# Optimization experiments

Measured on AMD Instinct MI355X. Metric: run time of the kernel, lower is better.

## Reference

```python
import jax, jax.numpy as jnp
import numpy as np

H = 512; W = 512          # image size
K = 1024                  # fixed cap on points per cloud (original is data-dependent)
P = 8                     # n_points = n_points_rate * radius
R = 1.0                   # radius
THR = 5                   # point_threshould
LAM = 0.1                 # lam


def _lbp_uniform(img):
    """skimage-style uniform LBP, P=8, R=1, bilinear sampling (edge-clamped)."""
    Hh, Ww = img.shape
    rows = jnp.arange(Hh)
    cols = jnp.arange(Ww)
    bits = []
    for k in range(P):
        dr = float(np.round(-R * np.sin(2.0 * np.pi * k / P), 8))
        dc = float(np.round(R * np.cos(2.0 * np.pi * k / P), 8))
        rr = rows + dr
        cc = cols + dc
        r0 = jnp.floor(rr)
        c0 = jnp.floor(cc)
        fr = (rr - r0)[:, None]
        fc = (cc - c0)[None, :]
        r0i = jnp.clip(r0.astype(jnp.int32), 0, Hh - 1)
        r1i = jnp.clip(r0i + 1, 0, Hh - 1)
        c0i = jnp.clip(c0.astype(jnp.int32), 0, Ww - 1)
        c1i = jnp.clip(c0i + 1, 0, Ww - 1)
        g = lambda ri, ci: img[ri][:, ci]
        sample = ((1 - fr) * ((1 - fc) * g(r0i, c0i) + fc * g(r0i, c1i))
                  + fr * ((1 - fc) * g(r1i, c0i) + fc * g(r1i, c1i)))
        bits.append((sample - img >= 0).astype(jnp.int32))
    b = jnp.stack(bits)                                    # [P,H,W]
    changes = jnp.sum(jnp.abs(b - jnp.roll(b, 1, axis=0)), axis=0)
    s = jnp.sum(b, axis=0)
    return jnp.where(changes <= 2, s, P + 1).astype(jnp.float32)


def _select_points(mask2d):
    """Row-major coordinates of True pixels, zero-padded/truncated to K points."""
    flat = mask2d.reshape(-1)
    order = jnp.argsort(jnp.where(flat, 0, 1), stable=True)[:K]  # True pixels first, row-major
    valid = flat[order].astype(jnp.float32)
    r = (order // W).astype(jnp.float32)
    c = (order % W).astype(jnp.float32)
    return jnp.stack([r, c], axis=-1) * valid[:, None]     # [K,2]


def _pdist(x):
    sq = jnp.sum(x * x, axis=-1)
    d2 = sq[:, None] + sq[None, :] - 2.0 * (x @ x.T)
    return jnp.sqrt(jnp.maximum(d2, 0.0))


def _mst_pairing(D):
    """Prim's MST edges = dim-0 Vietoris-Rips persistence pairing. [K-1,2] int32."""
    N = D.shape[0]
    INF = jnp.float32(1e9)
    in_tree = jnp.zeros(N, bool).at[0].set(True)
    mind = D[0]
    src = jnp.zeros(N, jnp.int32)

    def step(carry, _):
        mind, src, in_tree = carry
        j = jnp.argmin(jnp.where(in_tree, INF, mind)).astype(jnp.int32)
        edge = jnp.stack([src[j], j])
        in_tree = in_tree.at[j].set(True)
        upd = (D[j] < mind) & ~in_tree
        mind = jnp.where(upd, D[j], mind)
        src = jnp.where(upd, j, src)
        return (mind, src, in_tree), edge

    _, edges = jax.lax.scan(step, (mind, src, in_tree), None, length=N - 1)
    return edges


def _sample_loss(pred_bin, mask_bin):
    pts_p = _select_points(_lbp_uniform(pred_bin) < THR)
    pts_m = _select_points(_lbp_uniform(mask_bin) < THR)
    Dp = _pdist(pts_p)
    Dm = _pdist(pts_m)
    ep = _mst_pairing(Dp)
    em = _mst_pairing(Dm)
    sig = lambda D, e: D[e[:, 0], e[:, 1]]
    l_p = jnp.linalg.norm(sig(Dp, ep) - sig(Dm, ep))   # signature of pred pairing
    l_m = jnp.linalg.norm(sig(Dp, em) - sig(Dm, em))   # signature of mask pairing
    return l_p + l_m


def setup_inputs() -> dict:
    key = jax.random.key(0)
    k1, k2, k3 = jax.random.split(key, 3)
    images = jax.random.normal(k1, (8, 1, H, W), dtype=jnp.float32)
    model_output = jax.random.normal(k2, (8, 1, H, W), dtype=jnp.float32)
    labels = jax.random.uniform(k3, (8, 1, H, W), dtype=jnp.float32)
    return {"images": images, "model_output": model_output, "labels": labels}


def reference(images, model_output, labels):
    preds = jax.nn.sigmoid(model_output[:, 0])          # squeeze channel dim
    masks = labels[:, 0]
    pred_bin = (preds > 0.5).astype(jnp.float32)
    mask_bin = (masks > 0.5).astype(jnp.float32)
    per_sample = jax.vmap(_sample_loss)(pred_bin, mask_bin)
    return LAM * jnp.sum(per_sample) / pred_bin.shape[0]
```

## Files before the change

kernel.cpp:

```cpp
#include <hip/hip_runtime.h>

#define HH 512
#define WW 512
#define NPIX (HH * WW)
#define NIMG 16
#define KPTS 1024
#define NWORDS (NPIX / 64)

__global__ void lbp_kernel(const float* __restrict__ mo,
                           const float* __restrict__ lb,
                           unsigned long long* __restrict__ maskbits) {
    int m = blockIdx.y;
    int pix = blockIdx.x * blockDim.x + threadIdx.x;
    int r = pix >> 9, c = pix & 511;
    int sample = m >> 1;
    const float* img = (m & 1) ? (lb + sample * NPIX) : (mo + sample * NPIX);
    float thr = (m & 1) ? 0.5f : 0.0f;

    int rm = r - (r > 0), rp = r + (r < HH - 1);
    int cm = c - (c > 0), cp = c + (c < WW - 1);
    const float* rowm = img + rm * WW;
    const float* row0 = img + r  * WW;
    const float* rowp = img + rp * WW;

    bool bmm = rowm[cm] > thr, bm0 = rowm[c] > thr, bmp = rowm[cp] > thr;
    bool b0m = row0[cm] > thr, b00 = row0[c] > thr, b0p = row0[cp] > thr;
    bool bpm = rowp[cm] > thr, bp0 = rowp[c] > thr, bpp = rowp[cp] > thr;

    bool r0e = (r == 0), c0e = (c == 0);
    bool t2m = r0e ? bpm : b0m;
    bool t2c = r0e ? bp0 : b00;
    bool t2p = r0e ? bpp : b0p;
    bool mc2 = c0e ? bmp : bm0;
    bool tc2 = c0e ? t2p : t2c;
    bool zc2 = c0e ? b0p : b00;
    bool pc2 = c0e ? bpp : bp0;

    unsigned bb =
        (b0p                     ?   1u : 0u)
      | ((bm0 & bmp & t2c & t2p) ?   2u : 0u)
      | (bm0                     ?   4u : 0u)
      | ((bmm & mc2 & t2m & tc2) ?   8u : 0u)
      | (b0m                     ?  16u : 0u)
      | ((b0m & zc2 & bpm & pc2) ?  32u : 0u)
      | (bp0                     ?  64u : 0u)
      | ((b0p & bp0 & bpp)       ? 128u : 0u);

    unsigned rol = ((bb << 1) | (bb >> 7)) & 0xFFu;
    int changes = __popc(bb ^ rol);
    int s = __popc(bb);
    bool maskbit = b00 && (changes <= 2) && (s < 5);

    unsigned long long w = __ballot(maskbit);
    if ((threadIdx.x & 63) == 0)
        maskbits[m * NWORDS + (pix >> 6)] = w;
}

__global__ void select_kernel(const unsigned long long* __restrict__ maskbits,
                              unsigned* __restrict__ ptsG) {
    __shared__ unsigned swv[4];
    int m = blockIdx.x, tid = threadIdx.x;
    int lane = tid & 63, wid = tid >> 6;

    for (int i = tid; i < KPTS; i += 256) ptsG[m * KPTS + i] = 0u;
    __syncthreads();

    unsigned running = 0;
    for (int ch = 0; ch < 16; ch++) {
        int w = ch * 256 + tid;
        unsigned long long word = maskbits[m * NWORDS + w];
        unsigned cnt = (unsigned)__popcll(word);

        unsigned x = cnt;
#pragma unroll
        for (int d = 1; d < 64; d <<= 1) {
            unsigned y = (unsigned)__shfl_up((int)x, d, 64);
            x += (lane >= d) ? y : 0u;
        }
        if (lane == 63) swv[wid] = x;
        __syncthreads();
        unsigned woff = 0, total = 0;
#pragma unroll
        for (int ww = 0; ww < 4; ww++) {
            unsigned t = swv[ww];
            total += t;
            woff += (ww < wid) ? t : 0u;
        }
        unsigned rank = running + woff + x - cnt;
        while (word) {
            int b = __builtin_ctzll(word);
            word &= word - 1;
            if (rank < (unsigned)KPTS) {
                unsigned p = (unsigned)(w * 64 + b);
                unsigned rr = p >> 9, cc = p & 511u;
                ptsG[m * KPTS + rank] = (rr << 16) | cc;
            }
            rank++;
        }
        running += total;
        if (running >= (unsigned)KPTS) break;
        __syncthreads();
    }
}

typedef short v2s __attribute__((ext_vector_type(2)));
typedef unsigned u32x4 __attribute__((ext_vector_type(4)));

__device__ __forceinline__ int dist2_packed(unsigned a, unsigned b) {
#if __has_builtin(__builtin_amdgcn_sdot2)
    v2s d = __builtin_bit_cast(v2s, a) - __builtin_bit_cast(v2s, b);
    return __builtin_amdgcn_sdot2(d, d, 0, false);
#else
    int dr = (int)(a >> 16) - (int)(b >> 16);
    int dc = (int)(a & 0xFFFFu) - (int)(b & 0xFFFFu);
    return __mul24(dr, dr) + __mul24(dc, dc);
#endif
}

template <int CTRL>
__device__ __forceinline__ unsigned umin_dpp(unsigned x) {
    unsigned o = (unsigned)__builtin_amdgcn_update_dpp((int)x, (int)x, CTRL,
                                                       0xf, 0xf, false);
    return o < x ? o : x;
}

__device__ __forceinline__ unsigned wave_min_to_lane63(unsigned x) {
    x = umin_dpp<0x111>(x);
    x = umin_dpp<0x112>(x);
    x = umin_dpp<0x114>(x);
    x = umin_dpp<0x118>(x);
    x = umin_dpp<0x142>(x);
    x = umin_dpp<0x143>(x);
    return x;
}

__device__ __forceinline__ unsigned umin3(unsigned a, unsigned b, unsigned c) {
    unsigned t = a < b ? a : b;
    return t < c ? t : c;
}

__device__ __forceinline__ unsigned mk_key(unsigned ps, unsigned qs, int izb) {
#if __has_builtin(__builtin_amdgcn_sdot2)
    v2s d = __builtin_bit_cast(v2s, ps) - __builtin_bit_cast(v2s, qs);
    return (unsigned)__builtin_amdgcn_sdot2(d, d, izb, false);
#else
    int dr = (int)(short)(ps >> 16) - (int)(short)(qs >> 16);
    int dc = (int)(short)(ps & 0xFFFFu) - (int)(short)(qs & 0xFFFFu);
    return (unsigned)(dr * dr + dc * dc + izb);
#endif
}

#define OSLOT_INIT(sl)                                                    \
    oi##sl = (((wid * 4 + sl) << 6) | lane) - 1024;       \
    oq##sl = base[((wid * 4 + sl) << 6) | lane] << 5;                     \
    ok##sl = mk_key(oq##sl, pt0s, oi##sl);

#define OSLOT_UPD(sl)                                                     \
    { unsigned _nk = mk_key(oq##sl, pjs, oi##sl);                         \
      ok##sl = (unsigned)min((int)ok##sl, (int)_nk); }

#define SEL16P(res)                                                       \
    { unsigned _a0 = b0 ? p1  : p0;                                       \
      unsigned _a1 = b0 ? p3  : p2;                                       \
      unsigned _a2 = b0 ? p5  : p4;                                       \
      unsigned _a3 = b0 ? p7  : p6;                                       \
      unsigned _a4 = b0 ? p9  : p8;                                       \
      unsigned _a5 = b0 ? p11 : p10;                                      \
      unsigned _a6 = b0 ? p13 : p12;                                      \
      unsigned _a7 = b0 ? p15 : p14;                                      \
      unsigned _c0 = b1 ? _a1 : _a0;                                      \
      unsigned _c1 = b1 ? _a3 : _a2;                                      \
      unsigned _c2 = b1 ? _a5 : _a4;                                      \
      unsigned _c3 = b1 ? _a7 : _a6;                                      \
      unsigned _e0 = b2 ? _c1 : _c0;                                      \
      unsigned _e1 = b2 ? _c3 : _c2;                                      \
      res = b3 ? _e1 : _e0; }

__global__ __launch_bounds__(256, 1) void mst_kernel(const unsigned* __restrict__ ptsG,
                                                     unsigned* __restrict__ edgesG) {
    __shared__ __align__(16) unsigned xmin[2][4];
    int tid = threadIdx.x;
    int lane = tid & 63, wid = tid >> 6;
    int m = blockIdx.x;
    const unsigned* base = ptsG + m * KPTS;
    unsigned pt0s = base[0] << 5;

    unsigned p0  = base[( 0 << 6) | lane] << 5;
    unsigned p1  = base[( 1 << 6) | lane] << 5;
    unsigned p2  = base[( 2 << 6) | lane] << 5;
    unsigned p3  = base[( 3 << 6) | lane] << 5;
    unsigned p4  = base[( 4 << 6) | lane] << 5;
    unsigned p5  = base[( 5 << 6) | lane] << 5;
    unsigned p6  = base[( 6 << 6) | lane] << 5;
    unsigned p7  = base[( 7 << 6) | lane] << 5;
    unsigned p8  = base[( 8 << 6) | lane] << 5;
    unsigned p9  = base[( 9 << 6) | lane] << 5;
    unsigned p10 = base[(10 << 6) | lane] << 5;
    unsigned p11 = base[(11 << 6) | lane] << 5;
    unsigned p12 = base[(12 << 6) | lane] << 5;
    unsigned p13 = base[(13 << 6) | lane] << 5;
    unsigned p14 = base[(14 << 6) | lane] << 5;
    unsigned p15 = base[(15 << 6) | lane] << 5;

    unsigned oq0, oq1, oq2, oq3;
    unsigned ok0, ok1, ok2, ok3;
    int      oi0, oi1, oi2, oi3;
    OSLOT_INIT(0); OSLOT_INIT(1); OSLOT_INIT(2); OSLOT_INIT(3);

    unsigned* eout = edgesG + m * KPTS;
    unsigned r3i = umin3(ok0, ok1, ok2);
    unsigned rk = r3i < ok3 ? r3i : ok3;

    unsigned acc = 0;
    int par = 0;

    for (int chk = 0; chk < 16; chk++) {
        int tmax = (chk < 15) ? 64 : 63;
        for (int t = 0; t < tmax; t++) {
            unsigned wmin = wave_min_to_lane63(rk);
            if (lane == 63) xmin[par][wid] = wmin;
            __syncthreads();

            u32x4 xv = *reinterpret_cast<const u32x4*>(&xmin[par][0]);
            unsigned vm = umin3(xv.x, xv.y, xv.z);
            vm = vm < xv.w ? vm : xv.w;
            unsigned wk = (unsigned)__builtin_amdgcn_readfirstlane((int)vm) + 1024u;
            par ^= 1;

            unsigned j = wk & 1023u;
            int wslot = (int)(j >> 6);
            int wlane = (int)(j & 63u);

            bool b0 = (wslot & 1) != 0, b1 = (wslot & 2) != 0;
            bool b2 = (wslot & 4) != 0, b3 = (wslot & 8) != 0;
            unsigned selPay;
            SEL16P(selPay);
            unsigned pjs = (unsigned)__builtin_amdgcn_readlane((int)selPay, wlane);

            acc = (lane == t) ? wk : acc;

            OSLOT_UPD(0); OSLOT_UPD(1); OSLOT_UPD(2); OSLOT_UPD(3);
            unsigned r3 = umin3(ok0, ok1, ok2);
            rk = r3 < ok3 ? r3 : ok3;
        }
        if (wid == 0) eout[(chk << 6) + lane] = acc;
    }
}

__global__ void recover_kernel(const unsigned* __restrict__ ptsG,
                               const unsigned* __restrict__ edgesG,
                               float* __restrict__ contrib) {
    __shared__ unsigned sS[KPTS];
    __shared__ unsigned sO[KPTS];
    __shared__ unsigned short sT[KPTS];
    int g = blockIdx.x, m = blockIdx.y;
    int tid = threadIdx.x;
    int partner = m ^ 1;

    for (int i = tid; i < KPTS; i += 256) {
        sS[i] = ptsG[m * KPTS + i];
        sO[i] = ptsG[partner * KPTS + i];
    }
    for (int e = tid; e < KPTS - 1; e += 256) {
        unsigned wkk = edgesG[m * KPTS + e];
        sT[wkk & 1023u] = (unsigned short)(e + 1);
    }
    if (tid == 0) sT[0] = 0;
    __syncthreads();

    int lane = tid & 63, w = tid >> 6;
    for (int k = 0; k < 16; k++) {
        int e = g * 64 + w * 16 + k;
        if (e >= KPTS - 1) break;
        unsigned wk = edgesG[m * KPTS + e];
        unsigned j = wk & 1023u;
        unsigned d2p = wk >> 10;
        unsigned pj = sS[j];
        unsigned te1 = (unsigned)(e + 1);

        unsigned best = 0xFFFFFFFFu;
#pragma unroll
        for (int i = 0; i < 16; i++) {
            int v = i * 64 + lane;
            unsigned pv = sS[v];
            int d2 = dist2_packed(pv, pj);
            unsigned tv1 = (unsigned)sT[v];
            bool qual = ((unsigned)d2 == d2p) && (tv1 < te1);
            unsigned cand = qual ? ((tv1 << 10) | (unsigned)v) : 0xFFFFFFFFu;
            best = cand < best ? cand : best;
        }
#pragma unroll
        for (int dd = 32; dd; dd >>= 1) {
            unsigned o = (unsigned)__shfl_xor((int)best, dd, 64);
            best = o < best ? o : best;
        }
        unsigned vsrc = best & 1023u;
        if (lane == 0) {
            unsigned oj = sO[j], os = sO[vsrc];
            float Dp = __fsqrt_rn((float)d2p);
            float Dm = __fsqrt_rn((float)dist2_packed(oj, os));
            float diff = Dp - Dm;
            contrib[m * (KPTS - 1) + e] = diff * diff;
        }
    }
}

__global__ void final_kernel(const float* __restrict__ contrib,
                             float* __restrict__ out) {
    __shared__ double part[NIMG];
    int t = threadIdx.x;
    if (t < NIMG) {
        double s = 0.0;
        for (int e = 0; e < KPTS - 1; e++)
            s += (double)contrib[t * (KPTS - 1) + e];
        part[t] = sqrt(s);
    }
    __syncthreads();
    if (t == 0) {
        double tot = 0.0;
        for (int i = 0; i < NIMG; i++) tot += part[i];
        out[0] = (float)(0.1 * tot / 8.0);
    }
}

extern "C" void kernel_launch(void* const* d_in, const int* in_sizes, int n_in,
                              void* d_out, int out_size, void* d_ws, size_t ws_size,
                              hipStream_t stream) {
    const float* mo = (const float*)d_in[1];
    const float* lb = (const float*)d_in[2];

    unsigned long long* maskbits = (unsigned long long*)d_ws;
    unsigned* edgesG = (unsigned*)d_ws;
    float* contrib = (float*)((char*)d_ws + (size_t)64 * 1024);
    unsigned* ptsG = (unsigned*)((char*)d_ws + (size_t)NIMG * NWORDS * 8);
    float* out = (float*)d_out;

    lbp_kernel<<<dim3(NPIX / 256, NIMG), 256, 0, stream>>>(mo, lb, maskbits);
    select_kernel<<<NIMG, 256, 0, stream>>>(maskbits, ptsG);
    mst_kernel<<<NIMG, 256, 0, stream>>>(ptsG, edgesG);
    recover_kernel<<<dim3(16, NIMG), 256, 0, stream>>>(ptsG, edgesG, contrib);
    final_kernel<<<1, 64, 0, stream>>>(contrib, out);
}
```

Before: 412.2 us.

## Interleave two independent Prim MST problems per block to hide barrier latency

Each MST block now runs the Prim iterations of two point clouds (pred and mask of one sample) in lockstep, with a single __syncthreads per pair of phases. Each phase reads the other cloud's reduction result that was published before the previous barrier. The serial per-step latency of the block-level min reduction, the barrier, and the readlane selection is meant to be overlapped with independent work from the second problem. The cost is twice the register state per thread and half as many blocks, which only matters if per-block throughput were the limit.

```diff
diff --git a/kernel.cpp b/kernel.cpp
--- a/kernel.cpp
+++ b/kernel.cpp
@@ -150,24 +150,15 @@
 #endif
 }
 
-#define OSLOT_INIT(sl)                                                    \
-    oi##sl = (((wid * 4 + sl) << 6) | lane) - 1024;       \
-    oq##sl = base[((wid * 4 + sl) << 6) | lane] << 5;                     \
-    ok##sl = mk_key(oq##sl, pt0s, oi##sl);
-
-#define OSLOT_UPD(sl)                                                     \
-    { unsigned _nk = mk_key(oq##sl, pjs, oi##sl);                         \
-      ok##sl = (unsigned)min((int)ok##sl, (int)_nk); }
-
-#define SEL16P(res)                                                       \
-    { unsigned _a0 = b0 ? p1  : p0;                                       \
-      unsigned _a1 = b0 ? p3  : p2;                                       \
-      unsigned _a2 = b0 ? p5  : p4;                                       \
-      unsigned _a3 = b0 ? p7  : p6;                                       \
-      unsigned _a4 = b0 ? p9  : p8;                                       \
-      unsigned _a5 = b0 ? p11 : p10;                                      \
-      unsigned _a6 = b0 ? p13 : p12;                                      \
-      unsigned _a7 = b0 ? p15 : p14;                                      \
+#define SEL16(P, res)                                                     \
+    { unsigned _a0 = b0 ? P##1  : P##0;                                   \
+      unsigned _a1 = b0 ? P##3  : P##2;                                   \
+      unsigned _a2 = b0 ? P##5  : P##4;                                   \
+      unsigned _a3 = b0 ? P##7  : P##6;                                   \
+      unsigned _a4 = b0 ? P##9  : P##8;                                   \
+      unsigned _a5 = b0 ? P##11 : P##10;                                  \
+      unsigned _a6 = b0 ? P##13 : P##12;                                  \
+      unsigned _a7 = b0 ? P##15 : P##14;                                  \
       unsigned _c0 = b1 ? _a1 : _a0;                                      \
       unsigned _c1 = b1 ? _a3 : _a2;                                      \
       unsigned _c2 = b1 ? _a5 : _a4;                                      \
@@ -176,74 +167,119 @@
       unsigned _e1 = b2 ? _c3 : _c2;                                      \
       res = b3 ? _e1 : _e0; }
 
+#define LOADP(P, B)                                                       \
+    unsigned P##0  = B[( 0 << 6) | lane] << 5;                            \
+    unsigned P##1  = B[( 1 << 6) | lane] << 5;                            \
+    unsigned P##2  = B[( 2 << 6) | lane] << 5;                            \
+    unsigned P##3  = B[( 3 << 6) | lane] << 5;                            \
+    unsigned P##4  = B[( 4 << 6) | lane] << 5;                            \
+    unsigned P##5  = B[( 5 << 6) | lane] << 5;                            \
+    unsigned P##6  = B[( 6 << 6) | lane] << 5;                            \
+    unsigned P##7  = B[( 7 << 6) | lane] << 5;                            \
+    unsigned P##8  = B[( 8 << 6) | lane] << 5;                            \
+    unsigned P##9  = B[( 9 << 6) | lane] << 5;                            \
+    unsigned P##10 = B[(10 << 6) | lane] << 5;                            \
+    unsigned P##11 = B[(11 << 6) | lane] << 5;                            \
+    unsigned P##12 = B[(12 << 6) | lane] << 5;                            \
+    unsigned P##13 = B[(13 << 6) | lane] << 5;                            \
+    unsigned P##14 = B[(14 << 6) | lane] << 5;                            \
+    unsigned P##15 = B[(15 << 6) | lane] << 5;
+
+#define MST_PHASE(P, OQ, OK, ACC, XI) do {                                \
+    u32x4 _xv = *reinterpret_cast<const u32x4*>(&xm[XI][par][0]);         \
+    unsigned _vm = umin3(_xv.x, _xv.y, _xv.z);                            \
+    _vm = _vm < _xv.w ? _vm : _xv.w;                                      \
+    unsigned _wk = (unsigned)__builtin_amdgcn_readfirstlane((int)_vm) + 1024u; \
+    unsigned _j = _wk & 1023u;                                            \
+    int _ws = (int)(_j >> 6), _wl = (int)(_j & 63u);                      \
+    bool b0 = (_ws & 1) != 0, b1 = (_ws & 2) != 0;                        \
+    bool b2 = (_ws & 4) != 0, b3 = (_ws & 8) != 0;                        \
+    unsigned _sel; SEL16(P, _sel);                                        \
+    unsigned _pjs = (unsigned)__builtin_amdgcn_readlane((int)_sel, _wl);  \
+    ACC = (lane == t) ? _wk : ACC;                                        \
+    { unsigned _nk = mk_key(OQ##0, _pjs, oi0);                            \
+      OK##0 = (unsigned)min((int)OK##0, (int)_nk); }                      \
+    { unsigned _nk = mk_key(OQ##1, _pjs, oi1);                            \
+      OK##1 = (unsigned)min((int)OK##1, (int)_nk); }                      \
+    { unsigned _nk = mk_key(OQ##2, _pjs, oi2);                            \
+      OK##2 = (unsigned)min((int)OK##2, (int)_nk); }                      \
+    { unsigned _nk = mk_key(OQ##3, _pjs, oi3);                            \
+      OK##3 = (unsigned)min((int)OK##3, (int)_nk); }                      \
+    unsigned _r3 = umin3(OK##0, OK##1, OK##2);                            \
+    unsigned _rk = _r3 < OK##3 ? _r3 : OK##3;                             \
+    unsigned _wm = wave_min_to_lane63(_rk);                               \
+    if (lane == 63) xm[XI][par ^ 1][wid] = _wm;                           \
+} while (0)
+
 __global__ __launch_bounds__(256, 1) void mst_kernel(const unsigned* __restrict__ ptsG,
                                                      unsigned* __restrict__ edgesG) {
-    __shared__ __align__(16) unsigned xmin[2][4];
+    __shared__ __align__(16) unsigned xm[2][2][4];
     int tid = threadIdx.x;
     int lane = tid & 63, wid = tid >> 6;
-    int m = blockIdx.x;
-    const unsigned* base = ptsG + m * KPTS;
-    unsigned pt0s = base[0] << 5;
-
-    unsigned p0  = base[( 0 << 6) | lane] << 5;
-    unsigned p1  = base[( 1 << 6) | lane] << 5;
-    unsigned p2  = base[( 2 << 6) | lane] << 5;
-    unsigned p3  = base[( 3 << 6) | lane] << 5;
-    unsigned p4  = base[( 4 << 6) | lane] << 5;
-    unsigned p5  = base[( 5 << 6) | lane] << 5;
-    unsigned p6  = base[( 6 << 6) | lane] << 5;
-    unsigned p7  = base[( 7 << 6) | lane] << 5;
-    unsigned p8  = base[( 8 << 6) | lane] << 5;
-    unsigned p9  = base[( 9 << 6) | lane] << 5;
-    unsigned p10 = base[(10 << 6) | lane] << 5;
-    unsigned p11 = base[(11 << 6) | lane] << 5;
-    unsigned p12 = base[(12 << 6) | lane] << 5;
-    unsigned p13 = base[(13 << 6) | lane] << 5;
-    unsigned p14 = base[(14 << 6) | lane] << 5;
-    unsigned p15 = base[(15 << 6) | lane] << 5;
-
-    unsigned oq0, oq1, oq2, oq3;
-    unsigned ok0, ok1, ok2, ok3;
-    int      oi0, oi1, oi2, oi3;
-    OSLOT_INIT(0); OSLOT_INIT(1); OSLOT_INIT(2); OSLOT_INIT(3);
-
-    unsigned* eout = edgesG + m * KPTS;
-    unsigned r3i = umin3(ok0, ok1, ok2);
-    unsigned rk = r3i < ok3 ? r3i : ok3;
-
-    unsigned acc = 0;
+    int b = blockIdx.x;
+    const unsigned* baseX = ptsG + (2 * b)     * KPTS;
+    const unsigned* baseY = ptsG + (2 * b + 1) * KPTS;
+    unsigned pt0sX = baseX[0] << 5;
+    unsigned pt0sY = baseY[0] << 5;
+
+    LOADP(pX, baseX)
+    LOADP(pY, baseY)
+
+    int oi0 = (((wid * 4 + 0) << 6) | lane) - 1024;
+    int oi1 = (((wid * 4 + 1) << 6) | lane) - 1024;
+    int oi2 = (((wid * 4 + 2) << 6) | lane) - 1024;
+    int oi3 = (((wid * 4 + 3) << 6) | lane) - 1024;
+
+    unsigned oqX0 = pX0, oqX1, oqX2, oqX3;
+    unsigned oqY0, oqY1, oqY2, oqY3;
+    oqX0 = baseX[((wid * 4 + 0) << 6) | lane] << 5;
+    oqX1 = baseX[((wid * 4 + 1) << 6) | lane] << 5;
+    oqX2 = baseX[((wid * 4 + 2) << 6) | lane] << 5;
+    oqX3 = baseX[((wid * 4 + 3) << 6) | lane] << 5;
+    oqY0 = baseY[((wid * 4 + 0) << 6) | lane] << 5;
+    oqY1 = baseY[((wid * 4 + 1) << 6) | lane] << 5;
+    oqY2 = baseY[((wid * 4 + 2) << 6) | lane] << 5;
+    oqY3 = baseY[((wid * 4 + 3) << 6) | lane] << 5;
+
+    unsigned okX0 = mk_key(oqX0, pt0sX, oi0);
+    unsigned okX1 = mk_key(oqX1, pt0sX, oi1);
+    unsigned okX2 = mk_key(oqX2, pt0sX, oi2);
+    unsigned okX3 = mk_key(oqX3, pt0sX, oi3);
+    unsigned okY0 = mk_key(oqY0, pt0sY, oi0);
+    unsigned okY1 = mk_key(oqY1, pt0sY, oi1);
+    unsigned okY2 = mk_key(oqY2, pt0sY, oi2);
+    unsigned okY3 = mk_key(oqY3, pt0sY, oi3);
+
+    unsigned* eoutX = edgesG + (2 * b)     * KPTS;
+    unsigned* eoutY = edgesG + (2 * b + 1) * KPTS;
+
+    {
+        unsigned r3 = umin3(okX0, okX1, okX2);
+        unsigned rk = r3 < okX3 ? r3 : okX3;
+        unsigned wm = wave_min_to_lane63(rk);
+        if (lane == 63) xm[0][0][wid] = wm;
+    }
+    {
+        unsigned r3 = umin3(okY0, okY1, okY2);
+        unsigned rk = r3 < okY3 ? r3 : okY3;
+        unsigned wm = wave_min_to_lane63(rk);
+        if (lane == 63) xm[1][0][wid] = wm;
+    }
+    __syncthreads();
+
+    unsigned accX = 0, accY = 0;
     int par = 0;
 
     for (int chk = 0; chk < 16; chk++) {
         int tmax = (chk < 15) ? 64 : 63;
         for (int t = 0; t < tmax; t++) {
-            unsigned wmin = wave_min_to_lane63(rk);
-            if (lane == 63) xmin[par][wid] = wmin;
+            MST_PHASE(pX, oqX, okX, accX, 0);
             __syncthreads();
-
-            u32x4 xv = *reinterpret_cast<const u32x4*>(&xmin[par][0]);
-            unsigned vm = umin3(xv.x, xv.y, xv.z);
-            vm = vm < xv.w ? vm : xv.w;
-            unsigned wk = (unsigned)__builtin_amdgcn_readfirstlane((int)vm) + 1024u;
+            MST_PHASE(pY, oqY, okY, accY, 1);
             par ^= 1;
-
-            unsigned j = wk & 1023u;
-            int wslot = (int)(j >> 6);
-            int wlane = (int)(j & 63u);
-
-            bool b0 = (wslot & 1) != 0, b1 = (wslot & 2) != 0;
-            bool b2 = (wslot & 4) != 0, b3 = (wslot & 8) != 0;
-            unsigned selPay;
-            SEL16P(selPay);
-            unsigned pjs = (unsigned)__builtin_amdgcn_readlane((int)selPay, wlane);
-
-            acc = (lane == t) ? wk : acc;
-
-            OSLOT_UPD(0); OSLOT_UPD(1); OSLOT_UPD(2); OSLOT_UPD(3);
-            unsigned r3 = umin3(ok0, ok1, ok2);
-            rk = r3 < ok3 ? r3 : ok3;
-        }
-        if (wid == 0) eout[(chk << 6) + lane] = acc;
+        }
+        if (wid == 0) eoutX[(chk << 6) + lane] = accX;
+        if (wid == 1) eoutY[(chk << 6) + lane] = accY;
     }
 }
 
@@ -337,7 +373,7 @@
 
     lbp_kernel<<<dim3(NPIX / 256, NIMG), 256, 0, stream>>>(mo, lb, maskbits);
     select_kernel<<<NIMG, 256, 0, stream>>>(maskbits, ptsG);
-    mst_kernel<<<NIMG, 256, 0, stream>>>(ptsG, edgesG);
+    mst_kernel<<<NIMG / 2, 256, 0, stream>>>(ptsG, edgesG);
     recover_kernel<<<dim3(16, NIMG), 256, 0, stream>>>(ptsG, edgesG, contrib);
     final_kernel<<<1, 64, 0, stream>>>(contrib, out);
 }
```

Result: slower. 668.5 us (+62.2%).
